# Kernel tuning notes

Measured on AMD Instinct MI355X. Metric: run time of the kernel, lower is better.

## Reference

```python
import jax, jax.numpy as jnp
import numpy as np

D_MODEL = 1024
H = 16
D_K = D_MODEL // H
B = 4
S = 2048
NEG_INF = -1e9


def setup_inputs() -> dict:
    key = jax.random.key(0)
    ks = jax.random.split(key, 12)
    def lin(kw, kb):
        # torch nn.Linear default init: U(-1/sqrt(fan_in), 1/sqrt(fan_in))
        bound = 1.0 / np.sqrt(D_MODEL)
        w = jax.random.uniform(kw, (D_MODEL, D_MODEL), jnp.float32, -bound, bound)
        b = jax.random.uniform(kb, (D_MODEL,), jnp.float32, -bound, bound)
        return w, b
    wq_w, wq_b = lin(ks[0], ks[1])
    wk_w, wk_b = lin(ks[2], ks[3])
    wv_w, wv_b = lin(ks[4], ks[5])
    wo_w, wo_b = lin(ks[6], ks[7])
    Q = jax.random.normal(ks[8], (B, S, D_MODEL), jnp.float32)
    K = jax.random.normal(ks[9], (B, S, D_MODEL), jnp.float32)
    V = jax.random.normal(ks[10], (B, S, D_MODEL), jnp.float32)
    # causal additive mask, broadcastable to [B, H, S, S]
    causal = jnp.tril(jnp.ones((S, S), jnp.bool_))
    mask = jnp.where(causal, 0.0, NEG_INF).astype(jnp.float32)[None, None]
    return {"Q": Q, "K": K, "V": V, "mask": mask,
            "wq_w": wq_w, "wq_b": wq_b, "wk_w": wk_w, "wk_b": wk_b,
            "wv_w": wv_w, "wv_b": wv_b, "wo_w": wo_w, "wo_b": wo_b}


def _split_heads(x):
    b, s, _ = x.shape
    return x.reshape(b, s, H, D_K).transpose(0, 2, 1, 3)  # [b,h,s,dk]


def reference(Q, K, V, mask, wq_w, wq_b, wk_w, wk_b, wv_w, wv_b, wo_w, wo_b):
    # Linear projections (torch Linear: x @ W^T + b)
    q = _split_heads(Q @ wq_w.T + wq_b)
    k = _split_heads(K @ wk_w.T + wk_b)
    v = _split_heads(V @ wv_w.T + wv_b)
    scores = jnp.einsum("bhqd,bhkd->bhqk", q, k) / jnp.sqrt(jnp.float32(D_K))
    scores = scores + mask
    attn = jax.nn.softmax(scores, axis=-1)
    out = jnp.einsum("bhqk,bhkd->bhqd", attn, v)
    concat = out.transpose(0, 2, 1, 3).reshape(Q.shape[0], Q.shape[1], D_MODEL)
    return concat @ wo_w.T + wo_b
```

## Files before the change

kernel.cpp:

```cpp
#include <hip/hip_runtime.h>
#include <hip/hip_bf16.h>


typedef __attribute__((ext_vector_type(8))) short short8;
typedef __attribute__((ext_vector_type(8))) short bf16x8;
typedef __attribute__((ext_vector_type(4))) float f32x4;
typedef __attribute__((ext_vector_type(4))) unsigned uint4v;

__device__ __forceinline__ short f2bf(float f) {
    __hip_bfloat16 h = __float2bfloat16(f);
    return __builtin_bit_cast(short, h);
}
__device__ __forceinline__ f32x4 mfma16(bf16x8 a, bf16x8 b, f32x4 c) {
    return __builtin_amdgcn_mfma_f32_16x16x32_bf16(a, b, c, 0, 0, 0);
}
__device__ __forceinline__ void async_copy16(const void* g, void* l) {
    __builtin_amdgcn_global_load_lds(
        (const __attribute__((address_space(1))) unsigned int*)g,
        (__attribute__((address_space(3))) unsigned int*)l, 16, 0, 0);
}

__global__ __launch_bounds__(256) void convert_k(
    const float* __restrict__ wq, const float* __restrict__ wk,
    const float* __restrict__ wv, const float* __restrict__ wo,
    const float* __restrict__ bq, const float* __restrict__ bk,
    const float* __restrict__ bv, const float* __restrict__ bo,
    short* __restrict__ wqb, short* __restrict__ wkb,
    short* __restrict__ wvb, short* __restrict__ wob,
    float* __restrict__ bqo, float* __restrict__ bko,
    float* __restrict__ bvo, float* __restrict__ boo)
{
    const int gid = blockIdx.x * 256 + threadIdx.x;

    auto cv8 = [&](const float* src, short* dst, int i8) {
        const float* s = src + (size_t)i8 * 8;
        f32x4 a = *(const f32x4*)s;
        f32x4 b2 = *(const f32x4*)(s + 4);
        short8 o;
#pragma unroll
        for (int j = 0; j < 4; j++) { o[j] = f2bf(a[j]); o[4 + j] = f2bf(b2[j]); }
        *(short8*)(dst + (size_t)i8 * 8) = o;
    };

    cv8(wq, wqb, gid);
    cv8(wk, wkb, gid);
    cv8(wv, wvb, gid);
    cv8(wo, wob, gid);
    if (gid < 1024) {
        bqo[gid] = bq[gid];
        bko[gid] = bk[gid];
        bvo[gid] = bv[gid];
        boo[gid] = bo[gid];
    }
}

template<int MODE, int XF32>
__global__ __launch_bounds__(512) void gemm_k(const void* __restrict__ Xv,
                                              const short* __restrict__ W,
                                              const float* __restrict__ Bias,
                                              void* __restrict__ Ov,
                                              float alpha)
{
    __shared__ short As[128 * 64];
    __shared__ short Bs[128 * 64];
    const int tid = threadIdx.x;
    const int lane = tid & 63;
    const int w = tid >> 6;
    const int wr = (w >> 1) * 32;
    const int wc = (w & 1) * 64;
    const int lid = blockIdx.y * 8 + blockIdx.x;
    const int m0 = ((lid & 7) * 8 + ((lid >> 3) & 7)) * 128;
    const int n0 = (lid >> 6) * 128;
    const int l15 = lane & 15, l4 = lane >> 4;

    f32x4 acc[2][4];
#pragma unroll
    for (int i = 0; i < 2; i++)
#pragma unroll
        for (int j = 0; j < 4; j++) acc[i][j] = f32x4{0.f, 0.f, 0.f, 0.f};

    int srow[2], scol[2];
#pragma unroll
    for (int ii = 0; ii < 2; ++ii) {
        int L = ii * 512 + tid;
        srow[ii] = L >> 3;
        scol[ii] = ((L & 7) ^ ((L >> 3) & 7)) * 8;
    }

    for (int k0 = 0; k0 < 1024; k0 += 64) {
#pragma unroll
        for (int ii = 0; ii < 2; ++ii) {
            async_copy16(W + (size_t)(n0 + srow[ii]) * 1024 + k0 + scol[ii],
                         Bs + (ii * 512 + w * 64) * 8);
        }
        if constexpr (XF32 == 1) {
            const float* Xf = (const float*)Xv;
#pragma unroll
            for (int ii = 0; ii < 2; ++ii) {
                int L = ii * 512 + tid;
                const float* s = Xf + (size_t)(m0 + srow[ii]) * 1024 + k0 + scol[ii];
                f32x4 a = *(const f32x4*)s;
                f32x4 b2 = *(const f32x4*)(s + 4);
                short8 o;
#pragma unroll
                for (int j = 0; j < 4; j++) { o[j] = f2bf(a[j]); o[4 + j] = f2bf(b2[j]); }
                *(short8*)(As + L * 8) = o;
            }
        } else {
            const short* Xb = (const short*)Xv;
#pragma unroll
            for (int ii = 0; ii < 2; ++ii) {
                async_copy16(Xb + (size_t)(m0 + srow[ii]) * 1024 + k0 + scol[ii],
                             As + (ii * 512 + w * 64) * 8);
            }
        }
        __syncthreads();

        bf16x8 af[2][2], bfv[2][4];
#pragma unroll
        for (int kk = 0; kk < 2; kk++) {
#pragma unroll
            for (int i = 0; i < 2; i++) {
                int row = wr + i * 16 + l15;
                af[kk][i] = *(const bf16x8*)(As + row * 64 + (((kk * 4 + l4) ^ (row & 7)) * 8));
            }
#pragma unroll
            for (int j = 0; j < 4; j++) {
                int row = wc + j * 16 + l15;
                bfv[kk][j] = *(const bf16x8*)(Bs + row * 64 + (((kk * 4 + l4) ^ (row & 7)) * 8));
            }
        }
#pragma unroll
        for (int kk = 0; kk < 2; kk++)
#pragma unroll
            for (int i = 0; i < 2; i++)
#pragma unroll
                for (int j = 0; j < 4; j++) {
                    if (MODE == 2) acc[i][j] = mfma16(bfv[kk][j], af[kk][i], acc[i][j]);
                    else           acc[i][j] = mfma16(af[kk][i], bfv[kk][j], acc[i][j]);
                }
        __syncthreads();
    }

#pragma unroll
    for (int i = 0; i < 2; i++)
#pragma unroll
        for (int j = 0; j < 4; j++)
#pragma unroll
            for (int r = 0; r < 4; r++) {
                int gm, gn;
                if (MODE == 2) { gn = n0 + wc + j * 16 + l4 * 4 + r; gm = m0 + wr + i * 16 + l15; }
                else           { gm = m0 + wr + i * 16 + l4 * 4 + r; gn = n0 + wc + j * 16 + l15; }
                float v = (acc[i][j][r] + Bias[gn]) * alpha;
                if (MODE == 0) {
                    ((float*)Ov)[(size_t)gm * 1024 + gn] = v;
                } else {
                    int b = gm >> 11, s = gm & 2047, h = gn >> 6, d = gn & 63;
                    size_t idx;
                    if (MODE == 1) idx = (((size_t)(b * 16 + h)) * 2048 + s) * 64 + d;
                    else           idx = (((size_t)(b * 16 + h)) * 64 + d) * 2048 + s;
                    ((short*)Ov)[idx] = f2bf(v);
                }
            }
}

__global__ __launch_bounds__(512) void attn_k(const short* __restrict__ qh,
                                              const short* __restrict__ kh,
                                              const short* __restrict__ vt,
                                              short* __restrict__ ac)
{
    __shared__ short Kb[2][64 * 64];
    __shared__ short Vb[2][64 * 64];

    const int id = blockIdx.x;
    const int bh = id & 63;
    const int qt = 15 - (id >> 6);
    const int tid = threadIdx.x, lane = tid & 63, w = tid >> 6;
    const int l15 = lane & 15, l4 = lane >> 4;
    const size_t base = (size_t)bh * 2048 * 64;
    const int b = bh >> 4, h = bh & 15;

    const int qrow0 = qt * 128 + w * 16;
    const int cdiag = 2 * qt + (w >> 2);
    const int nkt = 2 * qt + 2;

    bf16x8 ones;
#pragma unroll
    for (int j = 0; j < 8; j++) ones[j] = (short)0x3F80;

    const int srow = tid >> 3;
    const int sg = (tid & 7) ^ (srow & 7);
    const short* kpp = kh + base + (size_t)srow * 64 + sg * 8;
    const short* vpp = vt + base + (size_t)srow * 2048 + sg * 8;

    bf16x8 qf[2];
#pragma unroll
    for (int kk = 0; kk < 2; kk++)
        qf[kk] = *(const bf16x8*)(qh + base + (size_t)(qrow0 + l15) * 64 + kk * 32 + l4 * 8);

    f32x4 o[4];
    f32x4 l_acc = f32x4{0.f, 0.f, 0.f, 0.f};
#pragma unroll
    for (int dt = 0; dt < 4; dt++) o[dt] = f32x4{0.f, 0.f, 0.f, 0.f};

    auto stage = [&](int kt, int buf) {
        async_copy16(kpp + (size_t)kt * 4096, &Kb[buf][w * 512]);
        async_copy16(vpp + (size_t)kt * 64,   &Vb[buf][w * 512]);
    };

    stage(0, 0);
    __syncthreads();

    for (int kt = 0; kt < nkt; ++kt) {
        const int cur = kt & 1;
        if (kt + 1 < nkt) stage(kt + 1, cur ^ 1);

        if (kt <= cdiag) {
            f32x4 st[4];
            const short* Kc = Kb[cur];
            const int sw = (l15 & 7) * 8;
            __builtin_amdgcn_s_setprio(1);
#pragma unroll
            for (int jt = 0; jt < 4; jt++) {
                const int rk = jt * 16 + l15;
                bf16x8 kf0 = *(const bf16x8*)(Kc + rk * 64 + ((l4 * 8) ^ sw));
                bf16x8 kf1 = *(const bf16x8*)(Kc + rk * 64 + ((32 + l4 * 8) ^ sw));
                st[jt] = mfma16(kf0, qf[0], f32x4{0.f, 0.f, 0.f, 0.f});
                st[jt] = mfma16(kf1, qf[1], st[jt]);
            }
            __builtin_amdgcn_s_setprio(0);

            if (kt == cdiag) {
                const int qg = qrow0 + l15;
#pragma unroll
                for (int jt = 0; jt < 4; jt++)
#pragma unroll
                    for (int r = 0; r < 4; r++) {
                        int jg = kt * 64 + jt * 16 + l4 * 4 + r;
                        if (jg > qg) st[jt][r] = -1e30f;
                    }
            }
#pragma unroll
            for (int jt = 0; jt < 4; jt++)
#pragma unroll
                for (int r = 0; r < 4; r++)
                    st[jt][r] = __builtin_amdgcn_exp2f(st[jt][r]);

            bf16x8 pf[2];
            unsigned xw[2][2], yw[2][2];
#pragma unroll
            for (int g = 0; g < 2; g++)
#pragma unroll
                for (int p = 0; p < 2; p++) {
                    unsigned a, bq;
                    asm("v_cvt_pk_bf16_f32 %0, %1, %2"
                        : "=v"(a) : "v"(st[2 * g][2 * p]), "v"(st[2 * g][2 * p + 1]));
                    asm("v_cvt_pk_bf16_f32 %0, %1, %2"
                        : "=v"(bq) : "v"(st[2 * g + 1][2 * p]), "v"(st[2 * g + 1][2 * p + 1]));
                    asm("v_permlane32_swap_b32 %0, %1" : "+v"(a), "+v"(bq));
                    asm("v_permlane16_swap_b32 %0, %1" : "+v"(a), "+v"(bq));
                    xw[g][p] = a; yw[g][p] = bq;
                }
#pragma unroll
            for (int kk = 0; kk < 2; kk++) {
                uint4v t{xw[kk][0], xw[kk][1], yw[kk][0], yw[kk][1]};
                pf[kk] = __builtin_bit_cast(bf16x8, t);
            }

            const short* Vc = Vb[cur];
            __builtin_amdgcn_s_setprio(1);
            l_acc = mfma16(pf[0], ones, l_acc);
            l_acc = mfma16(pf[1], ones, l_acc);
#pragma unroll
            for (int dt = 0; dt < 4; dt++) {
                const int rv = dt * 16 + l15;
                bf16x8 vf0 = *(const bf16x8*)(Vc + rv * 64 + ((l4 * 8) ^ sw));
                bf16x8 vf1 = *(const bf16x8*)(Vc + rv * 64 + ((32 + l4 * 8) ^ sw));
                o[dt] = mfma16(pf[0], vf0, o[dt]);
                o[dt] = mfma16(pf[1], vf1, o[dt]);
            }
            __builtin_amdgcn_s_setprio(0);
        }
        __syncthreads();
    }

#pragma unroll
    for (int r = 0; r < 4; r++) {
        float inv = 1.0f / l_acc[r];
        int qg = qrow0 + l4 * 4 + r;
#pragma unroll
        for (int dt = 0; dt < 4; dt++) {
            int d = dt * 16 + l15;
            ac[((size_t)(b * 2048 + qg)) * 1024 + h * 64 + d] = f2bf(o[dt][r] * inv);
        }
    }
}

extern "C" void kernel_launch(void* const* d_in, const int* in_sizes, int n_in,
                              void* d_out, int out_size, void* d_ws, size_t ws_size,
                              hipStream_t stream) {
    const float* Q    = (const float*)d_in[0];
    const float* K    = (const float*)d_in[1];
    const float* V    = (const float*)d_in[2];
    const float* wq_w = (const float*)d_in[4];
    const float* wq_b = (const float*)d_in[5];
    const float* wk_w = (const float*)d_in[6];
    const float* wk_b = (const float*)d_in[7];
    const float* wv_w = (const float*)d_in[8];
    const float* wv_b = (const float*)d_in[9];
    const float* wo_w = (const float*)d_in[10];
    const float* wo_b = (const float*)d_in[11];

    char* ws = (char*)d_ws;
    const size_t MB16 = (size_t)16 * 1024 * 1024;
    const size_t MB2  = (size_t)2 * 1024 * 1024;
    float* bq = (float*)(ws + 4096);
    float* bk = (float*)(ws + 8192);
    float* bv = (float*)(ws + 12288);
    float* bo = (float*)(ws + 16384);
    short* wqb = (short*)(ws + 65536);
    short* wkb = (short*)(ws + 65536 + MB2);
    short* wvb = (short*)(ws + 65536 + 2 * MB2);
    short* wob = (short*)(ws + 65536 + 3 * MB2);
    short* qh  = (short*)(ws + 65536 + 4 * MB2);
    short* kh  = (short*)(ws + 65536 + 4 * MB2 + MB16);
    short* vt  = (short*)(ws + 65536 + 4 * MB2 + 2 * MB16);
    short* ac  = (short*)(ws + 65536 + 4 * MB2 + 3 * MB16);

    convert_k<<<dim3(512), dim3(256), 0, stream>>>(
        wq_w, wk_w, wv_w, wo_w, wq_b, wk_b, wv_b, wo_b,
        wqb, wkb, wvb, wob, bq, bk, bv, bo);

    const float ALPHA_Q = 0.125f * 1.4426950408889634f;
    dim3 gg(8, 64), bb(512);
    gemm_k<1, 1><<<gg, bb, 0, stream>>>(Q, wqb, bq, qh, ALPHA_Q);
    gemm_k<1, 1><<<gg, bb, 0, stream>>>(K, wkb, bk, kh, 1.0f);
    gemm_k<2, 1><<<gg, bb, 0, stream>>>(V, wvb, bv, vt, 1.0f);

    attn_k<<<dim3(1024), bb, 0, stream>>>(qh, kh, vt, ac);

    gemm_k<0, 0><<<gg, bb, 0, stream>>>(ac, wob, bo, d_out, 1.0f);
}
```

Measured before the change: 147.3 us.

## Prefetch fp32 activations into registers and interleave causal attention tile order

In the projection GEMM that reads fp32 inputs, the next k-slice of X is now loaded into registers one iteration ahead, so global load latency overlaps the MFMA work of the current slice instead of stalling before the LDS store. The attention kernel also changes the query-tile order from strictly descending to an interleaved pattern that pairs heavy and light causal tiles within each group of blocks, to even out per-wave work across CUs. The prefetch costs extra VGPRs, which may reduce occupancy. The loop variable was renamed to avoid shadowing the new variable.

```diff
diff --git a/kernel.cpp b/kernel.cpp
--- a/kernel.cpp
+++ b/kernel.cpp
@@ -87,6 +87,17 @@
         scol[ii] = ((L & 7) ^ ((L >> 3) & 7)) * 8;
     }
 
+    f32x4 xpre[2][2];
+    if constexpr (XF32 == 1) {
+        const float* Xf = (const float*)Xv;
+#pragma unroll
+        for (int ii = 0; ii < 2; ++ii) {
+            const float* s = Xf + (size_t)(m0 + srow[ii]) * 1024 + scol[ii];
+            xpre[ii][0] = *(const f32x4*)s;
+            xpre[ii][1] = *(const f32x4*)(s + 4);
+        }
+    }
+
     for (int k0 = 0; k0 < 1024; k0 += 64) {
 #pragma unroll
         for (int ii = 0; ii < 2; ++ii) {
@@ -94,17 +105,25 @@
                          Bs + (ii * 512 + w * 64) * 8);
         }
         if constexpr (XF32 == 1) {
-            const float* Xf = (const float*)Xv;
 #pragma unroll
             for (int ii = 0; ii < 2; ++ii) {
                 int L = ii * 512 + tid;
-                const float* s = Xf + (size_t)(m0 + srow[ii]) * 1024 + k0 + scol[ii];
-                f32x4 a = *(const f32x4*)s;
-                f32x4 b2 = *(const f32x4*)(s + 4);
                 short8 o;
 #pragma unroll
-                for (int j = 0; j < 4; j++) { o[j] = f2bf(a[j]); o[4 + j] = f2bf(b2[j]); }
+                for (int j = 0; j < 4; j++) {
+                    o[j] = f2bf(xpre[ii][0][j]);
+                    o[4 + j] = f2bf(xpre[ii][1][j]);
+                }
                 *(short8*)(As + L * 8) = o;
+            }
+            if (k0 + 64 < 1024) {
+                const float* Xf = (const float*)Xv;
+#pragma unroll
+                for (int ii = 0; ii < 2; ++ii) {
+                    const float* s = Xf + (size_t)(m0 + srow[ii]) * 1024 + (k0 + 64) + scol[ii];
+                    xpre[ii][0] = *(const f32x4*)s;
+                    xpre[ii][1] = *(const f32x4*)(s + 4);
+                }
             }
         } else {
             const short* Xb = (const short*)Xv;
@@ -174,7 +193,9 @@
 
     const int id = blockIdx.x;
     const int bh = id & 63;
-    const int qt = 15 - (id >> 6);
+    const int g = id >> 6;
+    const int r4 = g & 3, q2 = g >> 2;
+    const int qt = (q2 == 0) ? 15 - r4 : (q2 == 1) ? r4 : (q2 == 2) ? 11 - r4 : 4 + r4;
     const int tid = threadIdx.x, lane = tid & 63, w = tid >> 6;
     const int l15 = lane & 15, l4 = lane >> 4;
     const size_t base = (size_t)bh * 2048 * 64;
@@ -249,17 +270,17 @@
             bf16x8 pf[2];
             unsigned xw[2][2], yw[2][2];
 #pragma unroll
-            for (int g = 0; g < 2; g++)
+            for (int gg = 0; gg < 2; gg++)
 #pragma unroll
                 for (int p = 0; p < 2; p++) {
                     unsigned a, bq;
                     asm("v_cvt_pk_bf16_f32 %0, %1, %2"
-                        : "=v"(a) : "v"(st[2 * g][2 * p]), "v"(st[2 * g][2 * p + 1]));
+                        : "=v"(a) : "v"(st[2 * gg][2 * p]), "v"(st[2 * gg][2 * p + 1]));
                     asm("v_cvt_pk_bf16_f32 %0, %1, %2"
-                        : "=v"(bq) : "v"(st[2 * g + 1][2 * p]), "v"(st[2 * g + 1][2 * p + 1]));
+                        : "=v"(bq) : "v"(st[2 * gg + 1][2 * p]), "v"(st[2 * gg + 1][2 * p + 1]));
                     asm("v_permlane32_swap_b32 %0, %1" : "+v"(a), "+v"(bq));
                     asm("v_permlane16_swap_b32 %0, %1" : "+v"(a), "+v"(bq));
-                    xw[g][p] = a; yw[g][p] = bq;
+                    xw[gg][p] = a; yw[gg][p] = bq;
                 }
 #pragma unroll
             for (int kk = 0; kk < 2; kk++) {
```

Result: slower. 155.8 us (+5.7%).

## Split attention blocks into 64-row halves with 256 threads and balanced tile order

Applied to the files above, without the earlier changes.

Each attention block now covers 64 query rows with 4 waves instead of 128 rows with 8 waves, and the grid doubles to 2048 blocks. Each half-block only walks the key tiles it needs, so the idle waves on the diagonal tile disappear. Query tiles are handed out in an interleaved heavy/light order to balance causal work across CUs. Every thread now issues two async copies per K/V tile, and each block stages the same K/V tiles for fewer query rows, which doubles K/V global traffic per unit of work.

```diff
diff --git a/kernel.cpp b/kernel.cpp
--- a/kernel.cpp
+++ b/kernel.cpp
@@ -164,7 +164,7 @@
             }
 }
 
-__global__ __launch_bounds__(512) void attn_k(const short* __restrict__ qh,
+__global__ __launch_bounds__(256) void attn_k(const short* __restrict__ qh,
                                               const short* __restrict__ kh,
                                               const short* __restrict__ vt,
                                               short* __restrict__ ac)
@@ -174,24 +174,33 @@
 
     const int id = blockIdx.x;
     const int bh = id & 63;
-    const int qt = 15 - (id >> 6);
+    const int half = (id >> 6) & 1;
+    const int g = id >> 7;
+    const int r4 = g & 3, q2 = g >> 2;
+    const int qt = (q2 == 0) ? 15 - r4 : (q2 == 1) ? r4 : (q2 == 2) ? 11 - r4 : 4 + r4;
     const int tid = threadIdx.x, lane = tid & 63, w = tid >> 6;
     const int l15 = lane & 15, l4 = lane >> 4;
     const size_t base = (size_t)bh * 2048 * 64;
     const int b = bh >> 4, h = bh & 15;
 
-    const int qrow0 = qt * 128 + w * 16;
-    const int cdiag = 2 * qt + (w >> 2);
-    const int nkt = 2 * qt + 2;
+    const int qrow0 = qt * 128 + half * 64 + w * 16;
+    const int nkt = 2 * qt + half + 1;
+    const int cdiag = nkt - 1;
 
     bf16x8 ones;
 #pragma unroll
     for (int j = 0; j < 8; j++) ones[j] = (short)0x3F80;
 
-    const int srow = tid >> 3;
-    const int sg = (tid & 7) ^ (srow & 7);
-    const short* kpp = kh + base + (size_t)srow * 64 + sg * 8;
-    const short* vpp = vt + base + (size_t)srow * 2048 + sg * 8;
+    const short* kp[2]; const short* vp[2]; int ldst[2];
+#pragma unroll
+    for (int ii = 0; ii < 2; ++ii) {
+        int L = ii * 256 + tid;
+        int row = L >> 3;
+        int gp = (L & 7) ^ (row & 7);
+        kp[ii] = kh + base + (size_t)row * 64 + gp * 8;
+        vp[ii] = vt + base + (size_t)row * 2048 + gp * 8;
+        ldst[ii] = (ii * 256 + w * 64) * 8;
+    }
 
     bf16x8 qf[2];
 #pragma unroll
@@ -204,8 +213,11 @@
     for (int dt = 0; dt < 4; dt++) o[dt] = f32x4{0.f, 0.f, 0.f, 0.f};
 
     auto stage = [&](int kt, int buf) {
-        async_copy16(kpp + (size_t)kt * 4096, &Kb[buf][w * 512]);
-        async_copy16(vpp + (size_t)kt * 64,   &Vb[buf][w * 512]);
+#pragma unroll
+        for (int ii = 0; ii < 2; ++ii) {
+            async_copy16(kp[ii] + (size_t)kt * 4096, &Kb[buf][0] + ldst[ii]);
+            async_copy16(vp[ii] + (size_t)kt * 64,   &Vb[buf][0] + ldst[ii]);
+        }
     };
 
     stage(0, 0);
@@ -215,7 +227,7 @@
         const int cur = kt & 1;
         if (kt + 1 < nkt) stage(kt + 1, cur ^ 1);
 
-        if (kt <= cdiag) {
+        {
             f32x4 st[4];
             const short* Kc = Kb[cur];
             const int sw = (l15 & 7) * 8;
@@ -249,17 +261,17 @@
             bf16x8 pf[2];
             unsigned xw[2][2], yw[2][2];
 #pragma unroll
-            for (int g = 0; g < 2; g++)
+            for (int gg = 0; gg < 2; gg++)
 #pragma unroll
                 for (int p = 0; p < 2; p++) {
                     unsigned a, bq;
                     asm("v_cvt_pk_bf16_f32 %0, %1, %2"
-                        : "=v"(a) : "v"(st[2 * g][2 * p]), "v"(st[2 * g][2 * p + 1]));
+                        : "=v"(a) : "v"(st[2 * gg][2 * p]), "v"(st[2 * gg][2 * p + 1]));
                     asm("v_cvt_pk_bf16_f32 %0, %1, %2"
-                        : "=v"(bq) : "v"(st[2 * g + 1][2 * p]), "v"(st[2 * g + 1][2 * p + 1]));
+                        : "=v"(bq) : "v"(st[2 * gg + 1][2 * p]), "v"(st[2 * gg + 1][2 * p + 1]));
                     asm("v_permlane32_swap_b32 %0, %1" : "+v"(a), "+v"(bq));
                     asm("v_permlane16_swap_b32 %0, %1" : "+v"(a), "+v"(bq));
-                    xw[g][p] = a; yw[g][p] = bq;
+                    xw[gg][p] = a; yw[gg][p] = bq;
                 }
 #pragma unroll
             for (int kk = 0; kk < 2; kk++) {
@@ -337,7 +349,7 @@
     gemm_k<1, 1><<<gg, bb, 0, stream>>>(K, wkb, bk, kh, 1.0f);
     gemm_k<2, 1><<<gg, bb, 0, stream>>>(V, wvb, bv, vt, 1.0f);
 
-    attn_k<<<dim3(1024), bb, 0, stream>>>(qh, kh, vt, ac);
+    attn_k<<<dim3(2048), dim3(256), 0, stream>>>(qh, kh, vt, ac);
 
     gemm_k<0, 0><<<gg, bb, 0, stream>>>(ac, wob, bo, d_out, 1.0f);
 }
```

New measurement: 163.6 us. 11.0% more time.
